# Kernel optimization log

Measured on AMD Instinct MI355X. Metric: run time of the kernel, lower is better.

The kernel has to match this reference:

```python
import jax, jax.numpy as jnp
import numpy as np
from jax import lax

N_PTS = 500000
CH = 64
GRID = 256
BN_EPS = 1e-5
A = -0.75  # torch bicubic coefficient


def setup_inputs() -> dict:
    key = jax.random.key(0)
    ks = jax.random.split(key, 10)
    coordinates = jax.random.uniform(ks[0], (N_PTS, 3), jnp.float32) * 2.0 - 1.0  # points in [-1,1]^3
    noise = jax.random.normal(ks[1], (3, N_PTS, 2), jnp.float32) * 0.01  # per-plane coord jitter (is_training)
    plane_x = jax.random.normal(ks[2], (1, CH, GRID, GRID), jnp.float32) * 0.001
    plane_y = jax.random.normal(ks[3], (1, CH, GRID, GRID), jnp.float32) * 0.001
    plane_z = jax.random.normal(ks[4], (1, CH, GRID, GRID), jnp.float32) * 0.001
    fan_in = CH * 9
    conv_w = jax.random.uniform(ks[5], (CH, CH, 3, 3), jnp.float32, -1.0, 1.0) / np.sqrt(fan_in)
    conv_b = jax.random.uniform(ks[6], (CH,), jnp.float32, -1.0, 1.0) / np.sqrt(fan_in)
    bn_gamma = jnp.ones((CH,), jnp.float32)
    bn_beta = jnp.zeros((CH,), jnp.float32)
    return {"coordinates": coordinates, "noise": noise, "plane_x": plane_x,
            "plane_y": plane_y, "plane_z": plane_z, "conv_w": conv_w,
            "conv_b": conv_b, "bn_gamma": bn_gamma, "bn_beta": bn_beta}


def res_block(p, conv_w, conv_b, gamma, beta):
    # conv3x3 stride2 pad1 -> BN (batch stats, training mode) -> relu, + avgpool3x3 s2 p1 (count_include_pad)
    y = lax.conv_general_dilated(p, conv_w, (2, 2), [(1, 1), (1, 1)],
                                 dimension_numbers=("NCHW", "OIHW", "NCHW"))
    y = y + conv_b[None, :, None, None]
    mu = jnp.mean(y, axis=(0, 2, 3), keepdims=True)
    var = jnp.var(y, axis=(0, 2, 3), keepdims=True)  # biased, as torch BN uses for normalization
    y = (y - mu) * lax.rsqrt(var + BN_EPS) * gamma[None, :, None, None] + beta[None, :, None, None]
    y = jax.nn.relu(y)
    pooled = lax.reduce_window(p, 0.0, lax.add, (1, 1, 3, 3), (1, 1, 2, 2),
                               [(0, 0), (0, 0), (1, 1), (1, 1)]) / 9.0
    return y + pooled


def cubic_weights(t):
    # torch cubic convolution weights, a=-0.75; t in [0,1). returns (4, M)
    t1 = t + 1.0
    w0 = ((A * t1 - 5 * A) * t1 + 8 * A) * t1 - 4 * A
    w1 = ((A + 2) * t - (A + 3)) * t * t + 1.0
    s = 1.0 - t
    w2 = ((A + 2) * s - (A + 3)) * s * s + 1.0
    w3 = 1.0 - w0 - w1 - w2
    return jnp.stack([w0, w1, w2, w3])


def sample_plane_bicubic(plane, grid):
    # plane: (C,H,W); grid: (M,2) with grid[:,0]->W axis, grid[:,1]->H axis (torch grid_sample layout)
    # bicubic, padding_mode='border', align_corners=True
    C, H, W = plane.shape
    gx = jnp.clip((grid[:, 0] + 1.0) * 0.5 * (W - 1), 0.0, W - 1.0)
    gy = jnp.clip((grid[:, 1] + 1.0) * 0.5 * (H - 1), 0.0, H - 1.0)
    x0f = jnp.floor(gx); y0f = jnp.floor(gy)
    tx = gx - x0f; ty = gy - y0f
    x0 = x0f.astype(jnp.int32); y0 = y0f.astype(jnp.int32)
    wx = cubic_weights(tx)  # (4,M)
    wy = cubic_weights(ty)  # (4,M)
    pl = jnp.transpose(plane, (1, 2, 0))  # (H,W,C)
    out = jnp.zeros((grid.shape[0], C), plane.dtype)
    for i in range(4):  # fixed 4x4 bicubic footprint
        yi = jnp.clip(y0 + (i - 1), 0, H - 1)
        for j in range(4):
            xi = jnp.clip(x0 + (j - 1), 0, W - 1)
            out = out + (wy[i] * wx[j])[:, None] * pl[yi, xi]
    return out  # (M,C)


def reference(coordinates, noise, plane_x, plane_y, plane_z, conv_w, conv_b, bn_gamma, bn_beta):
    bound = 1.0
    c = (coordinates + bound) / (2.0 * bound)  # (N,3) in [0,1] (fed to grid_sample as-is, faithful)
    px = res_block(plane_x, conv_w, conv_b, bn_gamma, bn_beta)[0]  # (C,128,128)
    py = res_block(plane_y, conv_w, conv_b, bn_gamma, bn_beta)[0]
    pz = res_block(plane_z, conv_w, conv_b, bn_gamma, bn_beta)[0]
    xy = sample_plane_bicubic(px, c[:, 0:2] + noise[0])
    yz = sample_plane_bicubic(py, c[:, 1:3] + noise[1])
    xz = sample_plane_bicubic(pz, c[:, 0:3:2] + noise[2])
    return xy + yz + xz  # (N,C)
```

## Files before the change

kernel.cpp:

```cpp
#include <hip/hip_runtime.h>
#include <hip/hip_fp16.h>

#define N_POINTS 500000
#define BN_EPS 1e-5f
#define A_COEF -0.75f

typedef __attribute__((ext_vector_type(8))) short short8;
typedef __attribute__((ext_vector_type(4))) float floatx4;
typedef unsigned short ushort_t;
typedef unsigned int uint_t;
typedef __attribute__((ext_vector_type(4))) uint_t uintx4;

#define WS_WBF_OFF    0
#define WS_CONV_OFF   18432
#define WS_SUM_OFF    (WS_CONV_OFF + 3145728)
#define WS_SUMSQ_OFF  (WS_SUM_OFF + 192)
#define WS_SCALE_OFF  (WS_SUMSQ_OFF + 192)
#define WS_SHIFT_OFF  (WS_SCALE_OFF + 192)
#define WS_PLANES_OFF (WS_SHIFT_OFF + 192)
#define WS_INBF_OFF   (WS_PLANES_OFF + 1572864)

__device__ __forceinline__ ushort_t f2bf(float f) {
  uint_t u = __float_as_uint(f);
  uint_t r = (u + 0x7fffu + ((u >> 16) & 1u)) >> 16;
  return (ushort_t)r;
}
__device__ __forceinline__ float bf2f(ushort_t u) {
  return __uint_as_float(((uint_t)u) << 16);
}

__global__ __launch_bounds__(256) void wprep_kernel(const float* __restrict__ w_in,
                                                    float* __restrict__ ws) {
  int i = blockIdx.x * 256 + threadIdx.x;
  if (i < 36864) {
    int ic = i & 63;
    int oc = (i >> 6) & 63;
    int kk = i >> 12;
    ((ushort_t*)(ws + WS_WBF_OFF))[i] = f2bf(w_in[(oc * 64 + ic) * 9 + kk]);
  }
  if (i < 384) ws[WS_SUM_OFF + i] = 0.0f;
}

__global__ __launch_bounds__(256) void transpose_kernel(const float* __restrict__ p0,
                                                        const float* __restrict__ p1,
                                                        const float* __restrict__ p2,
                                                        float* __restrict__ ws) {
  __shared__ float tile[64][65];
  const int xt = blockIdx.x, y = blockIdx.y, pl = blockIdx.z;
  const float* src = (pl == 0) ? p0 : ((pl == 1) ? p1 : p2);
  ushort_t* dst = (ushort_t*)(ws + WS_INBF_OFF) + pl * (256 * 256 * 64);
  const int t = threadIdx.x;
  const int x0 = xt * 64;
  for (int i = t; i < 4096; i += 256) {
    int c = i >> 6, x = i & 63;
    tile[x][c] = src[(c * 256 + y) * 256 + x0 + x];
  }
  __syncthreads();
  uint_t* du = (uint_t*)dst;
  for (int i = t; i < 2048; i += 256) {
    int x = i >> 5, cp = (i & 31) * 2;
    uint_t lo = f2bf(tile[x][cp]);
    uint_t hi = f2bf(tile[x][cp + 1]);
    du[((y * 256 + x0 + x) * 64 + cp) >> 1] = (hi << 16) | lo;
  }
}

__global__ __launch_bounds__(256) void conv_mfma_kernel(const float* __restrict__ ws_r,
                                                        float* __restrict__ ws) {
  const int xh = blockIdx.x, oy = blockIdx.y, pz = blockIdx.z;
  const int t = threadIdx.x;
  const int wv = t >> 6, lane = t & 63;
  const int mn = lane & 15;
  const int kg = lane >> 4;
  const int x0w = xh * 64 + wv * 16;

  const ushort_t* inb = (const ushort_t*)(ws_r + WS_INBF_OFF) + pz * (256 * 256 * 64);
  const ushort_t* wbf = (const ushort_t*)(ws_r + WS_WBF_OFF);

  floatx4 acc[4] = {{0.f,0.f,0.f,0.f},{0.f,0.f,0.f,0.f},{0.f,0.f,0.f,0.f},{0.f,0.f,0.f,0.f}};

  for (int ky = 0; ky < 3; ky++) {
    int y = 2 * oy - 1 + ky;
    if (y < 0) continue;
    const ushort_t* rowp = inb + y * (256 * 64);
    for (int kx = 0; kx < 3; kx++) {
      int xm = 2 * (x0w + mn) - 1 + kx;
      bool vx = xm >= 0;
      int xc = vx ? xm : 0;
      const ushort_t* abase = rowp + xc * 64 + kg * 8;
      const ushort_t* wbase = wbf + ((ky * 3 + kx) * 64 + mn) * 64 + kg * 8;
#pragma unroll
      for (int kc = 0; kc < 2; kc++) {
        union { int4 i4; short8 s8; } au;
        au.i4 = *reinterpret_cast<const int4*>(abase + kc * 32);
        if (!vx) au.i4 = make_int4(0, 0, 0, 0);
#pragma unroll
        for (int nt = 0; nt < 4; nt++) {
          union { int4 i4; short8 s8; } bu;
          bu.i4 = *reinterpret_cast<const int4*>(wbase + nt * 1024 + kc * 32);
          acc[nt] = __builtin_amdgcn_mfma_f32_16x16x32_bf16(au.s8, bu.s8, acc[nt], 0, 0, 0);
        }
      }
    }
  }
  float* cout = ws + WS_CONV_OFF + ((pz * 128 + oy) * 128 + x0w) * 64;
#pragma unroll
  for (int nt = 0; nt < 4; nt++) {
#pragma unroll
    for (int r = 0; r < 4; r++) {
      cout[(kg * 4 + r) * 64 + nt * 16 + mn] = acc[nt][r];
    }
  }

  float* sums  = ws + WS_SUM_OFF + pz * 64;
  float* sumsq = ws + WS_SUMSQ_OFF + pz * 64;
#pragma unroll
  for (int nt = 0; nt < 4; nt++) {
    float s = 0.f, s2 = 0.f;
#pragma unroll
    for (int r = 0; r < 4; r++) {
      float v = acc[nt][r];
      s += v;
      s2 = fmaf(v, v, s2);
    }
    s += __shfl_xor(s, 16, 64);  s2 += __shfl_xor(s2, 16, 64);
    s += __shfl_xor(s, 32, 64);  s2 += __shfl_xor(s2, 32, 64);
    if (kg == 0) {
      atomicAdd(&sums[nt * 16 + mn], s);
      atomicAdd(&sumsq[nt * 16 + mn], s2);
    }
  }
}

__global__ __launch_bounds__(256) void apply_kernel(float* __restrict__ ws,
                                                    const float* __restrict__ gamma,
                                                    const float* __restrict__ beta,
                                                    __half* __restrict__ planes) {
  int idx = blockIdx.x * 256 + threadIdx.x;
  int g = idx & 7;
  int p = (idx >> 3) & 16383;
  int pl = idx >> 17;
  int oy = p >> 7, ox = p & 127;
  int cb = g * 8;

  const float* conv = ws + WS_CONV_OFF;
  float4 a0 = *reinterpret_cast<const float4*>(conv + (size_t)idx * 8);
  float4 a1 = *reinterpret_cast<const float4*>(conv + (size_t)idx * 8 + 4);

  float sc[8], sh[8];
#pragma unroll
  for (int k = 0; k < 8; k++) {
    int c = cb + k;
    float mu = ws[WS_SUM_OFF + pl * 64 + c] * (1.0f / 16384.0f);
    float var = ws[WS_SUMSQ_OFF + pl * 64 + c] * (1.0f / 16384.0f) - mu * mu;
    var = fmaxf(var, 0.0f);
    float rstd = 1.0f / sqrtf(var + BN_EPS);
    float s = gamma[c] * rstd;
    sc[k] = s;
    sh[k] = beta[c] - mu * s;
  }

  const ushort_t* inb = (const ushort_t*)(ws + WS_INBF_OFF) + pl * (256 * 256 * 64);
  float ps[8];
#pragma unroll
  for (int k = 0; k < 8; k++) ps[k] = 0.0f;
#pragma unroll
  for (int r = 0; r < 3; r++) {
    int yy = 2 * oy - 1 + r;
    if (yy < 0) continue;
#pragma unroll
    for (int s = 0; s < 3; s++) {
      int xx = 2 * ox - 1 + s;
      if (xx < 0) continue;
      union { int4 i4; ushort_t u[8]; } ub;
      ub.i4 = *reinterpret_cast<const int4*>(inb + (yy * 256 + xx) * 64 + cb);
#pragma unroll
      for (int k = 0; k < 8; k++) ps[k] += bf2f(ub.u[k]);
    }
  }

  float v[8] = {a0.x, a0.y, a0.z, a0.w, a1.x, a1.y, a1.z, a1.w};
  union { int4 i4; __half h[8]; } ob;
#pragma unroll
  for (int k = 0; k < 8; k++) {
    float r = fmaxf(fmaf(v[k], sc[k], sh[k]), 0.0f) + ps[k] * (1.0f / 9.0f);
    ob.h[k] = __float2half(r);
  }
  *reinterpret_cast<int4*>(planes + (size_t)idx * 8) = ob.i4;
}

__device__ __forceinline__ void cubic_w(float t, float w[4]) {
  float t1 = t + 1.0f;
  w[0] = ((A_COEF * t1 - 5.0f * A_COEF) * t1 + 8.0f * A_COEF) * t1 - 4.0f * A_COEF;
  w[1] = ((A_COEF + 2.0f) * t - (A_COEF + 3.0f)) * t * t + 1.0f;
  float s = 1.0f - t;
  w[2] = ((A_COEF + 2.0f) * s - (A_COEF + 3.0f)) * s * s + 1.0f;
  w[3] = 1.0f - w[0] - w[1] - w[2];
}

__device__ __forceinline__ void gl8(uintx4& q0, uintx4& q1, uintx4& q2, uintx4& q3,
                                    uintx4& q4, uintx4& q5, uintx4& q6, uintx4& q7,
                                    uint_t o0, uint_t o1, uint_t o2, uint_t o3,
                                    uint_t o4, uint_t o5, uint_t o6, uint_t o7,
                                    const __half* base) {
  asm volatile(
      "global_load_dwordx4 %0, %8, %16\n\t"
      "global_load_dwordx4 %1, %9, %16\n\t"
      "global_load_dwordx4 %2, %10, %16\n\t"
      "global_load_dwordx4 %3, %11, %16\n\t"
      "global_load_dwordx4 %4, %12, %16\n\t"
      "global_load_dwordx4 %5, %13, %16\n\t"
      "global_load_dwordx4 %6, %14, %16\n\t"
      "global_load_dwordx4 %7, %15, %16"
      : "=&v"(q0), "=&v"(q1), "=&v"(q2), "=&v"(q3),
        "=&v"(q4), "=&v"(q5), "=&v"(q6), "=&v"(q7)
      : "v"(o0), "v"(o1), "v"(o2), "v"(o3),
        "v"(o4), "v"(o5), "v"(o6), "v"(o7),
        "s"(base));
}

__device__ __forceinline__ void fma_mix_tap(float& a0, float& a1, float& a2, float& a3,
                                            float& a4, float& a5, float& a6, float& a7,
                                            uint_t qx, uint_t qy, uint_t qz, uint_t qw,
                                            float w) {
  asm("v_fma_mix_f32 %0, %8, %12, %0 op_sel:[0,0,0] op_sel_hi:[1,0,0]\n\t"
      "v_fma_mix_f32 %1, %8, %12, %1 op_sel:[1,0,0] op_sel_hi:[1,0,0]\n\t"
      "v_fma_mix_f32 %2, %9, %12, %2 op_sel:[0,0,0] op_sel_hi:[1,0,0]\n\t"
      "v_fma_mix_f32 %3, %9, %12, %3 op_sel:[1,0,0] op_sel_hi:[1,0,0]\n\t"
      "v_fma_mix_f32 %4, %10, %12, %4 op_sel:[0,0,0] op_sel_hi:[1,0,0]\n\t"
      "v_fma_mix_f32 %5, %10, %12, %5 op_sel:[1,0,0] op_sel_hi:[1,0,0]\n\t"
      "v_fma_mix_f32 %6, %11, %12, %6 op_sel:[0,0,0] op_sel_hi:[1,0,0]\n\t"
      "v_fma_mix_f32 %7, %11, %12, %7 op_sel:[1,0,0] op_sel_hi:[1,0,0]"
      : "+v"(a0), "+v"(a1), "+v"(a2), "+v"(a3),
        "+v"(a4), "+v"(a5), "+v"(a6), "+v"(a7)
      : "v"(qx), "v"(qy), "v"(qz), "v"(qw), "v"(w));
}

__global__ __launch_bounds__(256) void sample_kernel(const float* __restrict__ coords,
                                                     const float* __restrict__ noise,
                                                     const __half* __restrict__ planes,
                                                     float* __restrict__ out) {
  const int t = threadIdx.x;
  const int wv = t >> 6, lane = t & 63;
  const int g = lane >> 3, l = lane & 7;
  const int n = blockIdx.x * 32 + wv * 8 + g;

  const float c0 = (coords[n * 3 + 0] + 1.0f) * 0.5f;
  const float c1 = (coords[n * 3 + 1] + 1.0f) * 0.5f;
  const float c2 = (coords[n * 3 + 2] + 1.0f) * 0.5f;

  float wxA[3][4], wyA[3][4];
  int ixA[3], iyA[3];
#pragma unroll
  for (int p = 0; p < 3; p++) {
    float u = (p == 1) ? c1 : c0;
    float v = (p == 0) ? c1 : c2;
    u += noise[(p * N_POINTS + n) * 2 + 0];
    v += noise[(p * N_POINTS + n) * 2 + 1];
    float gx = fminf(fmaxf(fmaf(u, 63.5f, 63.5f), 0.0f), 127.0f);
    float gy = fminf(fmaxf(fmaf(v, 63.5f, 63.5f), 0.0f), 127.0f);
    float x0f = floorf(gx), y0f = floorf(gy);
    cubic_w(gx - x0f, wxA[p]);
    cubic_w(gy - y0f, wyA[p]);
    ixA[p] = (int)x0f;
    iyA[p] = (int)y0f;
  }

  float a0 = 0.f, a1 = 0.f, a2 = 0.f, a3 = 0.f;
  float a4 = 0.f, a5 = 0.f, a6 = 0.f, a7 = 0.f;

#pragma unroll
  for (int p = 0; p < 3; p++) {
    const int ix = ixA[p], iy = iyA[p];
    const int rb = p * (128 * 128 * 64) + l * 8;
    int ro[4], xo[4];
#pragma unroll
    for (int i = 0; i < 4; i++) ro[i] = rb + min(max(iy - 1 + i, 0), 127) * (128 * 64);
#pragma unroll
    for (int j = 0; j < 4; j++) xo[j] = min(max(ix - 1 + j, 0), 127) * 64;

    uint_t off[16];
#pragma unroll
    for (int i = 0; i < 4; i++)
#pragma unroll
      for (int j = 0; j < 4; j++) off[i * 4 + j] = (uint_t)(ro[i] + xo[j]) * 2u;

    uintx4 q0, q1, q2, q3, q4, q5, q6, q7, q8, q9, qa, qb, qc, qd, qe, qf;
    gl8(q0, q1, q2, q3, q4, q5, q6, q7,
        off[0], off[1], off[2], off[3], off[4], off[5], off[6], off[7], planes);
    gl8(q8, q9, qa, qb, qc, qd, qe, qf,
        off[8], off[9], off[10], off[11], off[12], off[13], off[14], off[15], planes);

    asm volatile("s_waitcnt vmcnt(8)");
    __builtin_amdgcn_sched_barrier(0);
    fma_mix_tap(a0,a1,a2,a3,a4,a5,a6,a7, q0.x,q0.y,q0.z,q0.w, wyA[p][0]*wxA[p][0]);
    fma_mix_tap(a0,a1,a2,a3,a4,a5,a6,a7, q1.x,q1.y,q1.z,q1.w, wyA[p][0]*wxA[p][1]);
    fma_mix_tap(a0,a1,a2,a3,a4,a5,a6,a7, q2.x,q2.y,q2.z,q2.w, wyA[p][0]*wxA[p][2]);
    fma_mix_tap(a0,a1,a2,a3,a4,a5,a6,a7, q3.x,q3.y,q3.z,q3.w, wyA[p][0]*wxA[p][3]);
    fma_mix_tap(a0,a1,a2,a3,a4,a5,a6,a7, q4.x,q4.y,q4.z,q4.w, wyA[p][1]*wxA[p][0]);
    fma_mix_tap(a0,a1,a2,a3,a4,a5,a6,a7, q5.x,q5.y,q5.z,q5.w, wyA[p][1]*wxA[p][1]);
    fma_mix_tap(a0,a1,a2,a3,a4,a5,a6,a7, q6.x,q6.y,q6.z,q6.w, wyA[p][1]*wxA[p][2]);
    fma_mix_tap(a0,a1,a2,a3,a4,a5,a6,a7, q7.x,q7.y,q7.z,q7.w, wyA[p][1]*wxA[p][3]);

    asm volatile("s_waitcnt vmcnt(0)");
    __builtin_amdgcn_sched_barrier(0);
    fma_mix_tap(a0,a1,a2,a3,a4,a5,a6,a7, q8.x,q8.y,q8.z,q8.w, wyA[p][2]*wxA[p][0]);
    fma_mix_tap(a0,a1,a2,a3,a4,a5,a6,a7, q9.x,q9.y,q9.z,q9.w, wyA[p][2]*wxA[p][1]);
    fma_mix_tap(a0,a1,a2,a3,a4,a5,a6,a7, qa.x,qa.y,qa.z,qa.w, wyA[p][2]*wxA[p][2]);
    fma_mix_tap(a0,a1,a2,a3,a4,a5,a6,a7, qb.x,qb.y,qb.z,qb.w, wyA[p][2]*wxA[p][3]);
    fma_mix_tap(a0,a1,a2,a3,a4,a5,a6,a7, qc.x,qc.y,qc.z,qc.w, wyA[p][3]*wxA[p][0]);
    fma_mix_tap(a0,a1,a2,a3,a4,a5,a6,a7, qd.x,qd.y,qd.z,qd.w, wyA[p][3]*wxA[p][1]);
    fma_mix_tap(a0,a1,a2,a3,a4,a5,a6,a7, qe.x,qe.y,qe.z,qe.w, wyA[p][3]*wxA[p][2]);
    fma_mix_tap(a0,a1,a2,a3,a4,a5,a6,a7, qf.x,qf.y,qf.z,qf.w, wyA[p][3]*wxA[p][3]);
  }

  float* op = out + (size_t)n * 64 + l * 8;
  *reinterpret_cast<float4*>(op)     = make_float4(a0, a1, a2, a3);
  *reinterpret_cast<float4*>(op + 4) = make_float4(a4, a5, a6, a7);
}

extern "C" void kernel_launch(void* const* d_in, const int* in_sizes, int n_in,
                              void* d_out, int out_size, void* d_ws, size_t ws_size,
                              hipStream_t stream) {
  const float* coords = (const float*)d_in[0];
  const float* noise  = (const float*)d_in[1];
  const float* px     = (const float*)d_in[2];
  const float* py     = (const float*)d_in[3];
  const float* pz     = (const float*)d_in[4];
  const float* conv_w = (const float*)d_in[5];
  const float* gamma  = (const float*)d_in[7];
  const float* beta   = (const float*)d_in[8];
  float* out = (float*)d_out;
  float* ws = (float*)d_ws;
  __half* planes = (__half*)(ws + WS_PLANES_OFF);

  wprep_kernel<<<144, 256, 0, stream>>>(conv_w, ws);
  transpose_kernel<<<dim3(4, 256, 3), 256, 0, stream>>>(px, py, pz, ws);
  conv_mfma_kernel<<<dim3(2, 128, 3), 256, 0, stream>>>(ws, ws);
  apply_kernel<<<1536, 256, 0, stream>>>(ws, gamma, beta, planes);
  sample_kernel<<<15625, 256, 0, stream>>>(coords, noise, planes, out);
}
```

Before: 383.0 us.

## Fuse prep stages into one cooperative kernel with grid syncs

Merges the weight prep, transpose, conv and BN-apply kernels into a single persistent cooperative kernel of 1024 blocks, using grid-wide syncs between stages. It falls back to the separate launches if the cooperative launch fails. The aim is to remove three kernel launch gaps and their tail bubbles. In exchange it adds grid-sync cost and limits parallelism, since stages now loop over virtual blocks and the conv stage leaves 256 blocks idle.

```diff
diff --git a/kernel.cpp b/kernel.cpp
--- a/kernel.cpp
+++ b/kernel.cpp
@@ -1,5 +1,6 @@
 #include <hip/hip_runtime.h>
 #include <hip/hip_fp16.h>
+#include <hip/hip_cooperative_groups.h>
 
 #define N_POINTS 500000
 #define BN_EPS 1e-5f
@@ -29,9 +30,9 @@
   return __uint_as_float(((uint_t)u) << 16);
 }
 
-__global__ __launch_bounds__(256) void wprep_kernel(const float* __restrict__ w_in,
-                                                    float* __restrict__ ws) {
-  int i = blockIdx.x * 256 + threadIdx.x;
+
+__device__ __forceinline__ void wprep_body(int i, const float* __restrict__ w_in,
+                                           float* __restrict__ ws) {
   if (i < 36864) {
     int ic = i & 63;
     int oc = (i >> 6) & 63;
@@ -41,15 +42,11 @@
   if (i < 384) ws[WS_SUM_OFF + i] = 0.0f;
 }
 
-__global__ __launch_bounds__(256) void transpose_kernel(const float* __restrict__ p0,
-                                                        const float* __restrict__ p1,
-                                                        const float* __restrict__ p2,
-                                                        float* __restrict__ ws) {
-  __shared__ float tile[64][65];
-  const int xt = blockIdx.x, y = blockIdx.y, pl = blockIdx.z;
-  const float* src = (pl == 0) ? p0 : ((pl == 1) ? p1 : p2);
+__device__ __forceinline__ void transpose_body(float (*tile)[65], int t,
+                                               int xt, int y, int pl,
+                                               const float* __restrict__ src,
+                                               float* __restrict__ ws) {
   ushort_t* dst = (ushort_t*)(ws + WS_INBF_OFF) + pl * (256 * 256 * 64);
-  const int t = threadIdx.x;
   const int x0 = xt * 64;
   for (int i = t; i < 4096; i += 256) {
     int c = i >> 6, x = i & 63;
@@ -63,19 +60,18 @@
     uint_t hi = f2bf(tile[x][cp + 1]);
     du[((y * 256 + x0 + x) * 64 + cp) >> 1] = (hi << 16) | lo;
   }
-}
-
-__global__ __launch_bounds__(256) void conv_mfma_kernel(const float* __restrict__ ws_r,
-                                                        float* __restrict__ ws) {
-  const int xh = blockIdx.x, oy = blockIdx.y, pz = blockIdx.z;
-  const int t = threadIdx.x;
+  __syncthreads();
+}
+
+__device__ __forceinline__ void conv_body(int t, int xh, int oy, int pz,
+                                          float* __restrict__ ws) {
   const int wv = t >> 6, lane = t & 63;
   const int mn = lane & 15;
   const int kg = lane >> 4;
   const int x0w = xh * 64 + wv * 16;
 
-  const ushort_t* inb = (const ushort_t*)(ws_r + WS_INBF_OFF) + pz * (256 * 256 * 64);
-  const ushort_t* wbf = (const ushort_t*)(ws_r + WS_WBF_OFF);
+  const ushort_t* inb = (const ushort_t*)(ws + WS_INBF_OFF) + pz * (256 * 256 * 64);
+  const ushort_t* wbf = (const ushort_t*)(ws + WS_WBF_OFF);
 
   floatx4 acc[4] = {{0.f,0.f,0.f,0.f},{0.f,0.f,0.f,0.f},{0.f,0.f,0.f,0.f},{0.f,0.f,0.f,0.f}};
 
@@ -111,7 +107,6 @@
       cout[(kg * 4 + r) * 64 + nt * 16 + mn] = acc[nt][r];
     }
   }
-
   float* sums  = ws + WS_SUM_OFF + pz * 64;
   float* sumsq = ws + WS_SUMSQ_OFF + pz * 64;
 #pragma unroll
@@ -132,11 +127,10 @@
   }
 }
 
-__global__ __launch_bounds__(256) void apply_kernel(float* __restrict__ ws,
-                                                    const float* __restrict__ gamma,
-                                                    const float* __restrict__ beta,
-                                                    __half* __restrict__ planes) {
-  int idx = blockIdx.x * 256 + threadIdx.x;
+__device__ __forceinline__ void apply_body(int idx, float* __restrict__ ws,
+                                           const float* __restrict__ gamma,
+                                           const float* __restrict__ beta,
+                                           __half* __restrict__ planes) {
   int g = idx & 7;
   int p = (idx >> 3) & 16383;
   int pl = idx >> 17;
@@ -187,6 +181,62 @@
     ob.h[k] = __float2half(r);
   }
   *reinterpret_cast<int4*>(planes + (size_t)idx * 8) = ob.i4;
+}
+
+__global__ __launch_bounds__(256, 4) void prep_all_kernel(const float* __restrict__ w_in,
+                                                          const float* __restrict__ p0,
+                                                          const float* __restrict__ p1,
+                                                          const float* __restrict__ p2,
+                                                          const float* __restrict__ gamma,
+                                                          const float* __restrict__ beta,
+                                                          float* __restrict__ ws,
+                                                          __half* __restrict__ planes) {
+  cooperative_groups::grid_group gg = cooperative_groups::this_grid();
+  __shared__ float tile[64][65];
+  const int bid = blockIdx.x, t = threadIdx.x;
+
+  wprep_body(bid * 256 + t, w_in, ws);
+  for (int vb = bid; vb < 3072; vb += 1024) {
+    const int xt = vb & 3, y = (vb >> 2) & 255, pl = vb >> 10;
+    const float* src = (pl == 0) ? p0 : ((pl == 1) ? p1 : p2);
+    transpose_body(tile, t, xt, y, pl, src, ws);
+  }
+  gg.sync();
+
+  if (bid < 768) {
+    conv_body(t, bid & 1, (bid >> 1) & 127, bid >> 8, ws);
+  }
+  gg.sync();
+
+  for (int vb = bid; vb < 1536; vb += 1024) {
+    apply_body(vb * 256 + t, ws, gamma, beta, planes);
+  }
+}
+
+__global__ __launch_bounds__(256) void wprep_kernel(const float* __restrict__ w_in,
+                                                    float* __restrict__ ws) {
+  wprep_body(blockIdx.x * 256 + threadIdx.x, w_in, ws);
+}
+
+__global__ __launch_bounds__(256) void transpose_kernel(const float* __restrict__ p0,
+                                                        const float* __restrict__ p1,
+                                                        const float* __restrict__ p2,
+                                                        float* __restrict__ ws) {
+  __shared__ float tile[64][65];
+  const int pl = blockIdx.z;
+  const float* src = (pl == 0) ? p0 : ((pl == 1) ? p1 : p2);
+  transpose_body(tile, threadIdx.x, blockIdx.x, blockIdx.y, pl, src, ws);
+}
+
+__global__ __launch_bounds__(256) void conv_mfma_kernel(float* __restrict__ ws) {
+  conv_body(threadIdx.x, blockIdx.x, blockIdx.y, blockIdx.z, ws);
+}
+
+__global__ __launch_bounds__(256) void apply_kernel(float* __restrict__ ws,
+                                                    const float* __restrict__ gamma,
+                                                    const float* __restrict__ beta,
+                                                    __half* __restrict__ planes) {
+  apply_body(blockIdx.x * 256 + threadIdx.x, ws, gamma, beta, planes);
 }
 
 __device__ __forceinline__ void cubic_w(float t, float w[4]) {
@@ -334,9 +384,15 @@
   float* ws = (float*)d_ws;
   __half* planes = (__half*)(ws + WS_PLANES_OFF);
 
-  wprep_kernel<<<144, 256, 0, stream>>>(conv_w, ws);
-  transpose_kernel<<<dim3(4, 256, 3), 256, 0, stream>>>(px, py, pz, ws);
-  conv_mfma_kernel<<<dim3(2, 128, 3), 256, 0, stream>>>(ws, ws);
-  apply_kernel<<<1536, 256, 0, stream>>>(ws, gamma, beta, planes);
+  void* args[] = {(void*)&conv_w, (void*)&px, (void*)&py, (void*)&pz,
+                  (void*)&gamma, (void*)&beta, (void*)&ws, (void*)&planes};
+  hipError_t err = hipLaunchCooperativeKernel((const void*)prep_all_kernel,
+                                              dim3(1024), dim3(256), args, 0, stream);
+  if (err != hipSuccess) {
+    wprep_kernel<<<144, 256, 0, stream>>>(conv_w, ws);
+    transpose_kernel<<<dim3(4, 256, 3), 256, 0, stream>>>(px, py, pz, ws);
+    conv_mfma_kernel<<<dim3(2, 128, 3), 256, 0, stream>>>(ws);
+    apply_kernel<<<1536, 256, 0, stream>>>(ws, gamma, beta, planes);
+  }
   sample_kernel<<<15625, 256, 0, stream>>>(coords, noise, planes, out);
 }
```

After: 604.8 us. 57.9% more time.
